# Optimization experiments

Hardware: AMD Instinct MI355X
Metric: run time of the kernel (lower is better)

Reference implementation:

```python
import jax, jax.numpy as jnp
import numpy as np

N = 50000      # nodes per graph
E = 800000     # edges per graph (avg degree 16)
IN = 128       # in_dim
OUT = 64       # out_dim
HEADS = 2      # second GCNConv out = OUT*HEADS = 128
FILL = 2.0     # improved=True self-loop weight


def setup_inputs():
    key = jax.random.key(0)
    ks = jax.random.split(key, 10)
    x1 = jax.random.normal(ks[0], (N, IN), jnp.float32)
    edge_index1 = jax.random.randint(ks[1], (2, E), 0, N)
    edge_weight1 = jax.random.uniform(ks[2], (E,), jnp.float32)
    x2 = jax.random.normal(ks[3], (N, IN), jnp.float32)
    edge_index2 = jax.random.randint(ks[4], (2, E), 0, N)
    edge_weight2 = jax.random.uniform(ks[5], (E,), jnp.float32)
    # shared tower params (source bug: gcn1 used for both inputs)
    W1 = jax.random.normal(ks[6], (IN, OUT), jnp.float32) / np.sqrt(IN)
    b1 = jnp.zeros((OUT,), jnp.float32)
    W2 = jax.random.normal(ks[7], (OUT, OUT * HEADS), jnp.float32) / np.sqrt(OUT)
    b2 = jnp.zeros((OUT * HEADS,), jnp.float32)
    return {"x1": x1, "edge_index1": edge_index1, "edge_weight1": edge_weight1,
            "x2": x2, "edge_index2": edge_index2, "edge_weight2": edge_weight2,
            "W1": W1, "b1": b1, "W2": W2, "b2": b2}


def _gcn_conv(x, src, dst, ew, W, b, n):
    # GCNConv(improved=True, add_self_loops=True, aggr='max')
    loop = jnp.arange(n)
    src = jnp.concatenate([src, loop])
    dst = jnp.concatenate([dst, loop])
    ew = jnp.concatenate([ew, jnp.full((n,), FILL, ew.dtype)])
    # symmetric gcn normalization
    deg = jax.ops.segment_sum(ew, dst, num_segments=n)
    dinv = jnp.where(deg > 0, jax.lax.rsqrt(jnp.maximum(deg, 1e-30)), 0.0)
    norm = dinv[src] * ew * dinv[dst]          # [E+N]
    h = x @ W                                   # [N, F_out]
    msg = norm[:, None] * h[src]                # [E+N, F_out] gathered messages
    out = jax.ops.segment_max(msg, dst, num_segments=n)  # scatter-max
    out = jnp.where(jnp.isfinite(out), out, 0.0)          # guard empty segments
    return out + b


def _tower(x, ei, ew, W1, b1, W2, b2):
    ew = jax.nn.relu(ew)
    h = _gcn_conv(x, ei[0], ei[1], ew, W1, b1, x.shape[0])
    return _gcn_conv(h, ei[0], ei[1], ew, W2, b2, x.shape[0])


def reference(x1, edge_index1, edge_weight1, x2, edge_index2, edge_weight2, W1, b1, W2, b2):
    g1 = _tower(x1, edge_index1, edge_weight1, W1, b1, W2, b2)
    g2 = _tower(x2, edge_index2, edge_weight2, W1, b1, W2, b2)
    return (g1, g2)
```

## Files before the change

### kernel.cpp

```cpp
#include <hip/hip_runtime.h>
#include <hip/hip_fp16.h>

static constexpr float FILLW = 2.0f;
static constexpr int BSH  = 6;
static constexpr int CAPB = 1792;
static constexpr int NPB  = 128;
static constexpr int EPT  = 8;

template<int F, int K, int TR, int KC, bool SCALE, typename OutT>
__device__ __forceinline__ void gemm_tile(const float* __restrict__ A,
        const float* __restrict__ W, OutT* __restrict__ C,
        const float* __restrict__ dv, int rb, int N,
        float* __restrict__ Ws, float* __restrict__ As){
    constexpr int NCH = K / KC;
    constexpr int TRp = TR + 4;
    constexpr int CG  = F / 8;
    constexpr int LPT = TR * KC / 1024;
    const int tid = threadIdx.x;
    for (int i = tid; i < K * F / 4; i += 256)
        ((float4*)Ws)[i] = ((const float4*)W)[i];
    const int tx = tid % CG, ty = tid / CG;
    const int c0 = tx * 8, r0 = ty * 8;

    float acc[8][8];
    #pragma unroll
    for (int i = 0; i < 8; ++i)
        #pragma unroll
        for (int j = 0; j < 8; ++j) acc[i][j] = 0.f;

    float4 st[LPT];
    auto gload = [&](int kc){
        #pragma unroll
        for (int l2 = 0; l2 < LPT; ++l2){
            int l = l2 * 256 + tid;
            int r = l / (KC / 4);
            int kk = (l % (KC / 4)) * 4;
            int ar = rb + r; if (ar >= N) ar = N - 1;
            st[l2] = *(const float4*)(A + (size_t)ar * K + kc * KC + kk);
        }
    };
    auto swrite = [&](int buf){
        float* p = As + buf * (KC * TRp);
        #pragma unroll
        for (int l2 = 0; l2 < LPT; ++l2){
            int l = l2 * 256 + tid;
            int r = l / (KC / 4);
            int kk = (l % (KC / 4)) * 4;
            p[(kk+0)*TRp + r] = st[l2].x;
            p[(kk+1)*TRp + r] = st[l2].y;
            p[(kk+2)*TRp + r] = st[l2].z;
            p[(kk+3)*TRp + r] = st[l2].w;
        }
    };

    gload(0); swrite(0);
    __syncthreads();
    for (int kc = 0; kc < NCH; ++kc){
        if (kc + 1 < NCH) gload(kc + 1);
        const float* Ab = As + (kc & 1) * (KC * TRp);
        #pragma unroll
        for (int j = 0; j < KC; ++j){
            const float* wrow = Ws + (kc * KC + j) * F + c0;
            float4 w0 = *(const float4*)(wrow);
            float4 w1 = *(const float4*)(wrow + 4);
            float4 a0 = *(const float4*)(Ab + j * TRp + r0);
            float4 a1 = *(const float4*)(Ab + j * TRp + r0 + 4);
            float av[8] = {a0.x,a0.y,a0.z,a0.w,a1.x,a1.y,a1.z,a1.w};
            float wvv[8] = {w0.x,w0.y,w0.z,w0.w,w1.x,w1.y,w1.z,w1.w};
            #pragma unroll
            for (int rr = 0; rr < 8; ++rr)
                #pragma unroll
                for (int cc = 0; cc < 8; ++cc)
                    acc[rr][cc] = fmaf(av[rr], wvv[cc], acc[rr][cc]);
        }
        if (kc + 1 < NCH){ swrite((kc + 1) & 1); __syncthreads(); }
    }
    #pragma unroll
    for (int rr = 0; rr < 8; ++rr){
        int row = rb + r0 + rr;
        if (row < N){
            float scv = 1.0f;
            if constexpr (SCALE) scv = dv[row];
            if constexpr (sizeof(OutT) == 2){
                __half2 o2[4];
                #pragma unroll
                for (int q = 0; q < 4; ++q)
                    o2[q] = __floats2half2_rn(acc[rr][2*q]*scv, acc[rr][2*q+1]*scv);
                *(float4*)((__half*)C + (size_t)row * F + c0) = *(float4*)o2;
            } else {
                float4 o0 = {acc[rr][0]*scv, acc[rr][1]*scv, acc[rr][2]*scv, acc[rr][3]*scv};
                float4 o1 = {acc[rr][4]*scv, acc[rr][5]*scv, acc[rr][6]*scv, acc[rr][7]*scv};
                *(float4*)((float*)C + (size_t)row * F + c0)     = o0;
                *(float4*)((float*)C + (size_t)row * F + c0 + 4) = o1;
            }
        }
    }
}

__global__ void __launch_bounds__(256) k_cg1(const float* __restrict__ x0,
        const float* __restrict__ x1, const float* __restrict__ W1,
        __half* __restrict__ h0, __half* __restrict__ h1,
        const int* __restrict__ src0, const int* __restrict__ src1,
        const int* __restrict__ dst0, const int* __restrict__ dst1,
        const float* __restrict__ ew0, const float* __restrict__ ew1,
        uint2* __restrict__ stage, int* __restrict__ gcnt,
        int N, int E, int BPT, int GB, int B1){
    __shared__ float Ws[64 * 128];
    __shared__ float As[2 * 8 * 260];
    if ((int)blockIdx.x < GB){
        int t  = (int)blockIdx.x / BPT;
        int rb = ((int)blockIdx.x - t * BPT) * 256;
        gemm_tile<64,128,256,8,false,__half>(t ? x1 : x0, W1, t ? h1 : h0,
                                             nullptr, rb, N, Ws, As);
        return;
    }
    int c = (int)blockIdx.x - GB;
    int t = c / NPB, blk = c % NPB;
    const int* src = t ? src1 : src0;
    const int* dst = t ? dst1 : dst0;
    const float* ew = t ? ew1 : ew0;
    uint2* stg = stage + (size_t)t * B1 * CAPB;
    int* gc = gcnt + t * B1;
    int* hist = (int*)Ws;
    const int tid = threadIdx.x;
    for (int i = tid; i < B1; i += 256) hist[i] = 0;
    __syncthreads();
    int per = (E + NPB - 1) / NPB;
    int e0 = blk * per;
    int e1 = e0 + per; if (e1 > E) e1 = E;
    for (int e = e0 + tid; e < e1; e += 256 * EPT){
        int dl[EPT];
        #pragma unroll
        for (int q = 0; q < EPT; ++q){ int ee = e + q*256; dl[q] = (ee < e1) ? dst[ee] : -1; }
        #pragma unroll
        for (int q = 0; q < EPT; ++q) if (dl[q] >= 0) atomicAdd(&hist[dl[q] >> BSH], 1);
    }
    __syncthreads();
    int rot = (blk * 193) % B1;
    for (int i = tid; i < B1; i += 256){
        int b = i + rot; if (b >= B1) b -= B1;
        int h = hist[b];
        hist[b] = h ? atomicAdd(&gc[b], h) : 0;
    }
    __syncthreads();
    for (int e = e0 + tid; e < e1; e += 256 * EPT){
        int dl[EPT], sl[EPT]; float wl[EPT];
        #pragma unroll
        for (int q = 0; q < EPT; ++q){
            int ee = e + q*256;
            if (ee < e1){ dl[q] = dst[ee]; sl[q] = src[ee]; wl[q] = fmaxf(ew[ee], 0.f); }
            else dl[q] = -1;
        }
        int r[EPT];
        #pragma unroll
        for (int q = 0; q < EPT; ++q)
            if (dl[q] >= 0) r[q] = atomicAdd(&hist[dl[q] >> BSH], 1);
        #pragma unroll
        for (int q = 0; q < EPT; ++q)
            if (dl[q] >= 0 && r[q] < CAPB)
                stg[(size_t)(dl[q] >> BSH) * CAPB + r[q]] =
                    make_uint2(__float_as_uint(wl[q]),
                               (unsigned)sl[q] | ((unsigned)(dl[q] & 63) << 16));
    }
}

__global__ void __launch_bounds__(256) k_pack(const uint2* __restrict__ stage,
        const int* __restrict__ gcnt, int* __restrict__ woff,
        float2* __restrict__ sn, float* __restrict__ dinv, int N, int E, int B1){
    const int bid = (int)blockIdx.x, tid = threadIdx.x;
    const int t = bid / B1, b = bid % B1;
    const uint2* stg = stage + (size_t)t * B1 * CAPB;
    const int* gc = gcnt + t * B1;
    __shared__ int   wsum[4];
    __shared__ int   nh[64];
    __shared__ float nw[64];
    __shared__ int   offs[64];
    int acc = 0;
    for (int i = tid; i < b; i += 256) acc += gc[i];
    #pragma unroll
    for (int o = 32; o; o >>= 1) acc += __shfl_down(acc, o);
    int lane = tid & 63, wv = tid >> 6;
    if (lane == 0) wsum[wv] = acc;
    if (tid < 64){ nh[tid] = 0; nw[tid] = 0.f; }
    __syncthreads();
    const int base = wsum[0] + wsum[1] + wsum[2] + wsum[3];
    int cnt = gc[b]; if (cnt > CAPB) cnt = CAPB;

    int   rr[7]; uint2 rec[7];
    #pragma unroll
    for (int q = 0; q < 7; ++q){
        int j = q * 256 + tid;
        if (j < cnt){
            uint2 v = stg[(size_t)b * CAPB + j];
            int nl = (v.y >> 16) & 63;
            rr[q] = atomicAdd(&nh[nl], 1);
            atomicAdd(&nw[nl], __uint_as_float(v.x));
            rec[q] = v;
        } else rec[q].y = 0xFFFFFFFFu;
    }
    __syncthreads();
    if (tid < 64){
        int v = nh[tid], sc = v;
        #pragma unroll
        for (int o = 1; o < 64; o <<= 1){ int u = __shfl_up(sc, o); if (tid >= o) sc += u; }
        offs[tid] = sc - v;
        int n = (b << BSH) + tid;
        if (n < N){
            woff[t * N + n] = base + sc - v;
            dinv[t * N + n] = rsqrtf(FILLW + nw[tid]);
        }
    }
    __syncthreads();
    float2* sno = sn + (size_t)t * E;
    #pragma unroll
    for (int q = 0; q < 7; ++q){
        if (rec[q].y != 0xFFFFFFFFu){
            int nl   = (int)((rec[q].y >> 16) & 63);
            int srcv = (int)(rec[q].y & 0xFFFFu);
            sno[(size_t)base + offs[nl] + rr[q]] =
                make_float2(__int_as_float(srcv), __uint_as_float(rec[q].x));
        }
    }
}

__global__ void __launch_bounds__(256) k_prescale(const float* __restrict__ dinv,
        __half* __restrict__ h1, int GN){
    int g = (int)blockIdx.x * 256 + threadIdx.x;
    float dv = (g < GN) ? dinv[g] : 0.f;
    int lane  = threadIdx.x & 63;
    int wbase = (int)blockIdx.x * 256 + (threadIdx.x & ~63);
    for (int r = 0; r < 64; ++r){
        int gr = wbase + r;
        float scv = __shfl(dv, r);
        if (gr < GN){
            __half* row = h1 + (size_t)gr * 64;
            row[lane] = __float2half(__half2float(row[lane]) * scv);
        }
    }
}

__global__ void __launch_bounds__(256) k_gemm2(const float* __restrict__ A0,
        const float* __restrict__ A1, const float* __restrict__ W,
        __half* __restrict__ C0, __half* __restrict__ C1,
        const float* __restrict__ dinv, int N, int BPT){
    __shared__ float Ws[64 * 128];
    __shared__ float As[2 * 16 * 132];
    int t  = (int)blockIdx.x / BPT;
    int rb = ((int)blockIdx.x - t * BPT) * 128;
    gemm_tile<128,64,128,16,true,__half>(t ? A1 : A0, W, t ? C1 : C0,
                                         dinv + t * N, rb, N, Ws, As);
}

template<int F, int UG>
__global__ void __launch_bounds__(256) k_agg(const int* __restrict__ woff,
        const float2* __restrict__ sn, const float* __restrict__ dinv,
        const __half* __restrict__ H0, const __half* __restrict__ H1,
        const float* __restrict__ bias, float* __restrict__ O0, float* __restrict__ O1,
        int N, int E, int BPT){
    constexpr int LPR = F / 8;
    constexpr int EG  = 64 / LPR;
    const int t = (int)blockIdx.x / BPT;
    const int lane = threadIdx.x & 63, wv = threadIdx.x >> 6;
    int n = ((int)blockIdx.x - t * BPT) * 4 + wv;
    if (n >= N) return;
    int g = t * N + n;
    int beg = woff[g];
    int end = (n == N - 1) ? E : woff[g + 1];
    int cnt = end - beg;
    const float2* st = sn + (size_t)t * E;
    const __half* H = t ? H1 : H0;
    float* O = t ? O1 : O0;
    const int fl = lane % LPR;
    const int eg = lane / LPR;

    float acc[8];
    {
        float4 hv = *(const float4*)(H + (size_t)n * F + fl * 8);
        const __half2* hp = (const __half2*)&hv;
        #pragma unroll
        for (int k = 0; k < 4; ++k){
            float2 f = __half22float2(hp[k]);
            acc[2*k]   = FILLW * f.x;
            acc[2*k+1] = FILLW * f.y;
        }
    }
    for (int base = 0; base < cnt; base += 64){
        int m = cnt - base; if (m > 64) m = 64;
        float2 er = make_float2(0.f, 0.f);
        if (lane < m) er = st[beg + base + lane];
        int   es = __float_as_int(er.x);
        float ew = er.y;
        for (int j = 0; j < m; j += EG * UG){
            int sl[UG]; float wl[UG]; float4 hv[UG];
            #pragma unroll
            for (int u = 0; u < UG; ++u){
                int jj = j + u * EG + eg; if (jj > m - 1) jj = m - 1;
                sl[u] = __shfl(es, jj);
                wl[u] = __shfl(ew, jj);
            }
            #pragma unroll
            for (int u = 0; u < UG; ++u)
                hv[u] = *(const float4*)(H + (size_t)sl[u] * F + fl * 8);
            #pragma unroll
            for (int u = 0; u < UG; ++u){
                const __half2* hp = (const __half2*)&hv[u];
                #pragma unroll
                for (int k = 0; k < 4; ++k){
                    float2 f = __half22float2(hp[k]);
                    acc[2*k]   = fmaxf(acc[2*k],   wl[u] * f.x);
                    acc[2*k+1] = fmaxf(acc[2*k+1], wl[u] * f.y);
                }
            }
        }
    }
    #pragma unroll
    for (int msk = LPR; msk < 64; msk <<= 1)
        #pragma unroll
        for (int k = 0; k < 8; ++k) acc[k] = fmaxf(acc[k], __shfl_xor(acc[k], msk));
    float di = dinv[g];
    if constexpr (F == 128){
        int f0 = fl * 8 + eg * 2;
        float2 bb = *(const float2*)(bias + f0);
        *(float2*)(O + (size_t)n * F + f0) =
            make_float2(di * acc[eg*2] + bb.x, di * acc[eg*2+1] + bb.y);
    } else {
        int f0 = fl * 8 + eg;
        O[(size_t)n * F + f0] = di * acc[eg] + bias[f0];
    }
}


extern "C" void kernel_launch(void* const* d_in, const int* in_sizes, int n_in,
                              void* d_out, int out_size, void* d_ws, size_t ws_size,
                              hipStream_t stream){
    const int E  = in_sizes[2];
    const int F1 = in_sizes[7];
    const int F2 = in_sizes[9];
    const int IN = in_sizes[6] / F1;
    const int N  = in_sizes[0] / IN;
    const int B1 = (N + 63) >> BSH;

    const float* W1 = (const float*)d_in[6];
    const float* b1 = (const float*)d_in[7];
    const float* W2 = (const float*)d_in[8];
    const float* b2 = (const float*)d_in[9];

    auto need = [&](int G){
        return (size_t)G * E * 8
             + (size_t)G * N * F2 * 2
             + (size_t)G * N * F1 * 4
             + (size_t)G * N * 8
             + (size_t)G * B1 * 4
             + 4096;
    };
    const int G = (ws_size >= need(2)) ? 2 : 1;

    float2* sn    = (float2*)d_ws;
    __half* hbuf  = (__half*)(sn + (size_t)G * E);
    float*  out1  = (float*)(hbuf + (size_t)G * N * F2);
    uint2*  stage = (uint2*)out1;
    float*  dinv  = out1 + (size_t)G * N * F1;
    int*    woff  = (int*)(dinv + (size_t)G * N);
    int*    gcnt  = woff + (size_t)G * N;

    const int BPT1 = (N + 255) / 256;
    const int BPT2 = (N + 127) / 128;
    const int ABT  = (N + 3) / 4;
    const int GB   = G * BPT1;

    for (int it = 0; it < 2; it += G){
        int t0 = it, t1 = (G == 2) ? it + 1 : it;
        const float* x0 = (const float*)d_in[t0*3], * x1 = (const float*)d_in[t1*3];
        const int* ei0 = (const int*)d_in[t0*3+1], * ei1 = (const int*)d_in[t1*3+1];
        const float* ew0 = (const float*)d_in[t0*3+2], * ew1 = (const float*)d_in[t1*3+2];
        const int* src0 = ei0, * dst0 = ei0 + E;
        const int* src1 = ei1, * dst1 = ei1 + E;
        __half* h1_0 = hbuf, * h1_1 = hbuf + (size_t)(G-1) * N * F1;
        __half* h2_0 = hbuf, * h2_1 = hbuf + (size_t)(G-1) * N * F2;
        float* o1_0 = out1, * o1_1 = out1 + (size_t)(G-1) * N * F1;
        float* go0 = (float*)d_out + (size_t)t0 * N * F2;
        float* go1 = (float*)d_out + (size_t)t1 * N * F2;

        hipMemsetAsync(gcnt, 0, (size_t)G * B1 * sizeof(int), stream);
        k_cg1<<<GB + G * NPB, 256, 0, stream>>>(x0, x1, W1, h1_0, h1_1,
                                                src0, src1, dst0, dst1, ew0, ew1,
                                                stage, gcnt, N, E, BPT1, GB, B1);
        k_pack<<<G * B1, 256, 0, stream>>>(stage, gcnt, woff, sn, dinv, N, E, B1);
        k_prescale<<<(G * N + 255) / 256, 256, 0, stream>>>(dinv, hbuf, G * N);
        k_agg<64,2><<<G * ABT, 256, 0, stream>>>(woff, sn, dinv, h1_0, h1_1, b1,
                                                 o1_0, o1_1, N, E, ABT);
        k_gemm2<<<G * BPT2, 256, 0, stream>>>(o1_0, o1_1, W2, h2_0, h2_1, dinv, N, BPT2);
        k_agg<128,4><<<G * ABT, 256, 0, stream>>>(woff, sn, dinv, h2_0, h2_1, b2,
                                                  go0, go1, N, E, ABT);
    }
}
```

Before: 357.4 us.

## Deterministic bucket scatter via scan, packed fp16 aggregation, fuse prescale into pack

Splits edge bucketing into a histogram pass, a per-bucket scan over per-block counts, and a separate scatter kernel, replacing global atomics and the memset so edge order is deterministic. The dinv prescale of h1 is fused into k_pack. Edge weights are stored as duplicated fp16 pairs and aggregation uses packed v_pk_mul/v_pk_max fp16 math. Layer-1 aggregation unroll rises from 2 to 4 and the histogram block count doubles. This adds two extra launches and lowers the precision of the max accumulation.

```diff
diff --git a/kernel.cpp b/kernel.cpp
--- a/kernel.cpp
+++ b/kernel.cpp
@@ -4,8 +4,15 @@
 static constexpr float FILLW = 2.0f;
 static constexpr int BSH  = 6;
 static constexpr int CAPB = 1792;
-static constexpr int NPB  = 128;
+static constexpr int NPB  = 256;
 static constexpr int EPT  = 8;
+
+__device__ __forceinline__ unsigned pk_mul(unsigned a, unsigned b){
+    unsigned r; asm("v_pk_mul_f16 %0, %1, %2" : "=v"(r) : "v"(a), "v"(b)); return r;
+}
+__device__ __forceinline__ unsigned pk_max(unsigned a, unsigned b){
+    unsigned r; asm("v_pk_max_f16 %0, %1, %2" : "=v"(r) : "v"(a), "v"(b)); return r;
+}
 
 template<int F, int K, int TR, int KC, bool SCALE, typename OutT>
 __device__ __forceinline__ void gemm_tile(const float* __restrict__ A,
@@ -100,10 +107,8 @@
 __global__ void __launch_bounds__(256) k_cg1(const float* __restrict__ x0,
         const float* __restrict__ x1, const float* __restrict__ W1,
         __half* __restrict__ h0, __half* __restrict__ h1,
-        const int* __restrict__ src0, const int* __restrict__ src1,
         const int* __restrict__ dst0, const int* __restrict__ dst1,
-        const float* __restrict__ ew0, const float* __restrict__ ew1,
-        uint2* __restrict__ stage, int* __restrict__ gcnt,
+        int* __restrict__ cnts,
         int N, int E, int BPT, int GB, int B1){
     __shared__ float Ws[64 * 128];
     __shared__ float As[2 * 8 * 260];
@@ -116,11 +121,7 @@
     }
     int c = (int)blockIdx.x - GB;
     int t = c / NPB, blk = c % NPB;
-    const int* src = t ? src1 : src0;
     const int* dst = t ? dst1 : dst0;
-    const float* ew = t ? ew1 : ew0;
-    uint2* stg = stage + (size_t)t * B1 * CAPB;
-    int* gc = gcnt + t * B1;
     int* hist = (int*)Ws;
     const int tid = threadIdx.x;
     for (int i = tid; i < B1; i += 256) hist[i] = 0;
@@ -136,13 +137,52 @@
         for (int q = 0; q < EPT; ++q) if (dl[q] >= 0) atomicAdd(&hist[dl[q] >> BSH], 1);
     }
     __syncthreads();
-    int rot = (blk * 193) % B1;
-    for (int i = tid; i < B1; i += 256){
-        int b = i + rot; if (b >= B1) b -= B1;
-        int h = hist[b];
-        hist[b] = h ? atomicAdd(&gc[b], h) : 0;
-    }
-    __syncthreads();
+    int* co = cnts + (size_t)(t * NPB + blk) * B1;
+    for (int i = tid; i < B1; i += 256) co[i] = hist[i];
+}
+
+__global__ void __launch_bounds__(64) k_scanR(int* __restrict__ cnts,
+        int* __restrict__ gcnt, int B1){
+    int bid = (int)blockIdx.x;
+    int t = bid / B1, b = bid % B1;
+    int lane = threadIdx.x;
+    int* cp = cnts + (size_t)t * NPB * B1 + b;
+    int x[4];
+    #pragma unroll
+    for (int j = 0; j < 4; ++j) x[j] = cp[(size_t)(lane * 4 + j) * B1];
+    int s = x[0] + x[1] + x[2] + x[3];
+    int sc = s;
+    #pragma unroll
+    for (int o = 1; o < 64; o <<= 1){ int u = __shfl_up(sc, o); if (lane >= o) sc += u; }
+    int e0 = sc - s;
+    int e1 = e0 + x[0], e2 = e1 + x[1], e3 = e2 + x[2];
+    cp[(size_t)(lane * 4 + 0) * B1] = e0;
+    cp[(size_t)(lane * 4 + 1) * B1] = e1;
+    cp[(size_t)(lane * 4 + 2) * B1] = e2;
+    cp[(size_t)(lane * 4 + 3) * B1] = e3;
+    if (lane == 63) gcnt[t * B1 + b] = sc;
+}
+
+__global__ void __launch_bounds__(256) k_scatter(const int* __restrict__ src0,
+        const int* __restrict__ src1,
+        const int* __restrict__ dst0, const int* __restrict__ dst1,
+        const float* __restrict__ ew0, const float* __restrict__ ew1,
+        const int* __restrict__ cnts, uint2* __restrict__ stage,
+        int N, int E, int B1){
+    __shared__ int hist[1024];
+    int c = (int)blockIdx.x;
+    int t = c / NPB, blk = c % NPB;
+    const int* src = t ? src1 : src0;
+    const int* dst = t ? dst1 : dst0;
+    const float* ew = t ? ew1 : ew0;
+    uint2* stg = stage + (size_t)t * B1 * CAPB;
+    const int* co = cnts + (size_t)(t * NPB + blk) * B1;
+    const int tid = threadIdx.x;
+    for (int i = tid; i < B1; i += 256) hist[i] = co[i];
+    __syncthreads();
+    int per = (E + NPB - 1) / NPB;
+    int e0 = blk * per;
+    int e1 = e0 + per; if (e1 > E) e1 = E;
     for (int e = e0 + tid; e < e1; e += 256 * EPT){
         int dl[EPT], sl[EPT]; float wl[EPT];
         #pragma unroll
@@ -166,7 +206,8 @@
 
 __global__ void __launch_bounds__(256) k_pack(const uint2* __restrict__ stage,
         const int* __restrict__ gcnt, int* __restrict__ woff,
-        float2* __restrict__ sn, float* __restrict__ dinv, int N, int E, int B1){
+        uint2* __restrict__ sn, float* __restrict__ dinv,
+        __half* __restrict__ h1, int N, int E, int B1){
     const int bid = (int)blockIdx.x, tid = threadIdx.x;
     const int t = bid / B1, b = bid % B1;
     const uint2* stg = stage + (size_t)t * B1 * CAPB;
@@ -175,6 +216,7 @@
     __shared__ int   nh[64];
     __shared__ float nw[64];
     __shared__ int   offs[64];
+    __shared__ float dvs[64];
     int acc = 0;
     for (int i = tid; i < b; i += 256) acc += gc[i];
     #pragma unroll
@@ -205,36 +247,36 @@
         for (int o = 1; o < 64; o <<= 1){ int u = __shfl_up(sc, o); if (tid >= o) sc += u; }
         offs[tid] = sc - v;
         int n = (b << BSH) + tid;
+        float dv = 0.f;
         if (n < N){
+            dv = rsqrtf(FILLW + nw[tid]);
             woff[t * N + n] = base + sc - v;
-            dinv[t * N + n] = rsqrtf(FILLW + nw[tid]);
-        }
-    }
-    __syncthreads();
-    float2* sno = sn + (size_t)t * E;
+            dinv[t * N + n] = dv;
+        }
+        dvs[tid] = dv;
+    }
+    __syncthreads();
+    uint2* sno = sn + (size_t)t * E;
     #pragma unroll
     for (int q = 0; q < 7; ++q){
         if (rec[q].y != 0xFFFFFFFFu){
             int nl   = (int)((rec[q].y >> 16) & 63);
-            int srcv = (int)(rec[q].y & 0xFFFFu);
+            unsigned srcv = rec[q].y & 0xFFFFu;
+            __half hw = __float2half(__uint_as_float(rec[q].x));
+            unsigned hu = (unsigned)__half_as_ushort(hw);
             sno[(size_t)base + offs[nl] + rr[q]] =
-                make_float2(__int_as_float(srcv), __uint_as_float(rec[q].x));
-        }
-    }
-}
-
-__global__ void __launch_bounds__(256) k_prescale(const float* __restrict__ dinv,
-        __half* __restrict__ h1, int GN){
-    int g = (int)blockIdx.x * 256 + threadIdx.x;
-    float dv = (g < GN) ? dinv[g] : 0.f;
-    int lane  = threadIdx.x & 63;
-    int wbase = (int)blockIdx.x * 256 + (threadIdx.x & ~63);
-    for (int r = 0; r < 64; ++r){
-        int gr = wbase + r;
-        float scv = __shfl(dv, r);
-        if (gr < GN){
-            __half* row = h1 + (size_t)gr * 64;
-            row[lane] = __float2half(__half2float(row[lane]) * scv);
+                make_uint2(srcv, hu | (hu << 16));
+        }
+    }
+    __half2* hb = (__half2*)(h1 + ((size_t)t * N + ((size_t)b << BSH)) * 64);
+    #pragma unroll
+    for (int j = 0; j < 8; ++j){
+        int idx = j * 256 + tid;
+        int r = idx >> 5, cc = idx & 31;
+        if ((b << BSH) + r < N){
+            float2 f = __half22float2(hb[r * 32 + cc]);
+            float dv = dvs[r];
+            hb[r * 32 + cc] = __floats2half2_rn(f.x * dv, f.y * dv);
         }
     }
 }
@@ -253,7 +295,7 @@
 
 template<int F, int UG>
 __global__ void __launch_bounds__(256) k_agg(const int* __restrict__ woff,
-        const float2* __restrict__ sn, const float* __restrict__ dinv,
+        const uint2* __restrict__ sn, const float* __restrict__ dinv,
         const __half* __restrict__ H0, const __half* __restrict__ H1,
         const float* __restrict__ bias, float* __restrict__ O0, float* __restrict__ O1,
         int N, int E, int BPT){
@@ -267,65 +309,67 @@
     int beg = woff[g];
     int end = (n == N - 1) ? E : woff[g + 1];
     int cnt = end - beg;
-    const float2* st = sn + (size_t)t * E;
+    const uint2* st = sn + (size_t)t * E;
     const __half* H = t ? H1 : H0;
     float* O = t ? O1 : O0;
     const int fl = lane % LPR;
     const int eg = lane / LPR;
 
-    float acc[8];
+    unsigned acc[4];
     {
         float4 hv = *(const float4*)(H + (size_t)n * F + fl * 8);
-        const __half2* hp = (const __half2*)&hv;
-        #pragma unroll
-        for (int k = 0; k < 4; ++k){
-            float2 f = __half22float2(hp[k]);
-            acc[2*k]   = FILLW * f.x;
-            acc[2*k+1] = FILLW * f.y;
-        }
+        const unsigned* hp = (const unsigned*)&hv;
+        const unsigned two2 = 0x40004000u;
+        #pragma unroll
+        for (int k = 0; k < 4; ++k) acc[k] = pk_mul(hp[k], two2);
     }
     for (int base = 0; base < cnt; base += 64){
         int m = cnt - base; if (m > 64) m = 64;
-        float2 er = make_float2(0.f, 0.f);
+        uint2 er = make_uint2(0u, 0u);
         if (lane < m) er = st[beg + base + lane];
-        int   es = __float_as_int(er.x);
-        float ew = er.y;
+        int es = (int)er.x;
+        int ep = (int)er.y;
         for (int j = 0; j < m; j += EG * UG){
-            int sl[UG]; float wl[UG]; float4 hv[UG];
+            int sl[UG], wl[UG]; float4 hv[UG];
             #pragma unroll
             for (int u = 0; u < UG; ++u){
                 int jj = j + u * EG + eg; if (jj > m - 1) jj = m - 1;
                 sl[u] = __shfl(es, jj);
-                wl[u] = __shfl(ew, jj);
+                wl[u] = __shfl(ep, jj);
             }
             #pragma unroll
             for (int u = 0; u < UG; ++u)
                 hv[u] = *(const float4*)(H + (size_t)sl[u] * F + fl * 8);
             #pragma unroll
             for (int u = 0; u < UG; ++u){
-                const __half2* hp = (const __half2*)&hv[u];
+                const unsigned* hp = (const unsigned*)&hv[u];
+                unsigned w2 = (unsigned)wl[u];
                 #pragma unroll
-                for (int k = 0; k < 4; ++k){
-                    float2 f = __half22float2(hp[k]);
-                    acc[2*k]   = fmaxf(acc[2*k],   wl[u] * f.x);
-                    acc[2*k+1] = fmaxf(acc[2*k+1], wl[u] * f.y);
-                }
+                for (int k = 0; k < 4; ++k)
+                    acc[k] = pk_max(acc[k], pk_mul(hp[k], w2));
             }
         }
     }
     #pragma unroll
     for (int msk = LPR; msk < 64; msk <<= 1)
         #pragma unroll
-        for (int k = 0; k < 8; ++k) acc[k] = fmaxf(acc[k], __shfl_xor(acc[k], msk));
+        for (int k = 0; k < 4; ++k){
+            unsigned o = (unsigned)__shfl_xor((int)acc[k], msk);
+            acc[k] = pk_max(acc[k], o);
+        }
     float di = dinv[g];
     if constexpr (F == 128){
         int f0 = fl * 8 + eg * 2;
+        float2 f = __half22float2(*(__half2*)&acc[eg]);
         float2 bb = *(const float2*)(bias + f0);
         *(float2*)(O + (size_t)n * F + f0) =
-            make_float2(di * acc[eg*2] + bb.x, di * acc[eg*2+1] + bb.y);
+            make_float2(di * f.x + bb.x, di * f.y + bb.y);
     } else {
         int f0 = fl * 8 + eg;
-        O[(size_t)n * F + f0] = di * acc[eg] + bias[f0];
+        unsigned av = acc[eg >> 1];
+        unsigned short hs = (unsigned short)((eg & 1) ? (av >> 16) : (av & 0xFFFFu));
+        float v = __half2float(__ushort_as_half(hs));
+        O[(size_t)n * F + f0] = di * v + bias[f0];
     }
 }
 
@@ -351,17 +395,19 @@
              + (size_t)G * N * F1 * 4
              + (size_t)G * N * 8
              + (size_t)G * B1 * 4
+             + (size_t)G * NPB * B1 * 4
              + 4096;
     };
     const int G = (ws_size >= need(2)) ? 2 : 1;
 
-    float2* sn    = (float2*)d_ws;
+    uint2*  sn    = (uint2*)d_ws;
     __half* hbuf  = (__half*)(sn + (size_t)G * E);
     float*  out1  = (float*)(hbuf + (size_t)G * N * F2);
     uint2*  stage = (uint2*)out1;
     float*  dinv  = out1 + (size_t)G * N * F1;
     int*    woff  = (int*)(dinv + (size_t)G * N);
     int*    gcnt  = woff + (size_t)G * N;
+    int*    cnts  = gcnt + (size_t)G * B1;
 
     const int BPT1 = (N + 255) / 256;
     const int BPT2 = (N + 127) / 128;
@@ -381,13 +427,13 @@
         float* go0 = (float*)d_out + (size_t)t0 * N * F2;
         float* go1 = (float*)d_out + (size_t)t1 * N * F2;
 
-        hipMemsetAsync(gcnt, 0, (size_t)G * B1 * sizeof(int), stream);
         k_cg1<<<GB + G * NPB, 256, 0, stream>>>(x0, x1, W1, h1_0, h1_1,
-                                                src0, src1, dst0, dst1, ew0, ew1,
-                                                stage, gcnt, N, E, BPT1, GB, B1);
-        k_pack<<<G * B1, 256, 0, stream>>>(stage, gcnt, woff, sn, dinv, N, E, B1);
-        k_prescale<<<(G * N + 255) / 256, 256, 0, stream>>>(dinv, hbuf, G * N);
-        k_agg<64,2><<<G * ABT, 256, 0, stream>>>(woff, sn, dinv, h1_0, h1_1, b1,
+                                                dst0, dst1, cnts, N, E, BPT1, GB, B1);
+        k_scanR<<<G * B1, 64, 0, stream>>>(cnts, gcnt, B1);
+        k_scatter<<<G * NPB, 256, 0, stream>>>(src0, src1, dst0, dst1, ew0, ew1,
+                                               cnts, stage, N, E, B1);
+        k_pack<<<G * B1, 256, 0, stream>>>(stage, gcnt, woff, sn, dinv, hbuf, N, E, B1);
+        k_agg<64,4><<<G * ABT, 256, 0, stream>>>(woff, sn, dinv, h1_0, h1_1, b1,
                                                  o1_0, o1_1, N, E, ABT);
         k_gemm2<<<G * BPT2, 256, 0, stream>>>(o1_0, o1_1, W2, h2_0, h2_1, dinv, N, BPT2);
         k_agg<128,4><<<G * ABT, 256, 0, stream>>>(woff, sn, dinv, h2_0, h2_1, b2,
```

Result: faster. 339.9 us (-4.9%).
